# Kernel tuning notes

Hardware: AMD Instinct MI355X
Metric: run time of the kernel (lower is better)

The kernel has to match this reference:

```python
import jax, jax.numpy as jnp
import numpy as np

DIM = 1024
CTX_DIM = 768
H = 16


def setup_inputs() -> dict:
    key = jax.random.key(0)
    k1, k2, k3, k4, k5 = jax.random.split(key, 5)
    x = jax.random.normal(k1, (2, 2048, DIM), dtype=jnp.float32)
    context = jax.random.normal(k2, (2, 2048, CTX_DIM), dtype=jnp.float32)
    # Linear weights stored as [in, out] (y = x @ W); no biases per module.
    s = 0.02
    Wq = jax.random.normal(k3, (DIM, DIM), dtype=jnp.float32) * s
    Wkv = jax.random.normal(k4, (CTX_DIM, 2 * DIM), dtype=jnp.float32) * s
    Wo = jax.random.normal(k5, (DIM, DIM), dtype=jnp.float32) * s
    return {"x": x, "context": context, "Wq": Wq, "Wkv": Wkv, "Wo": Wo}


def reference(x, context, Wq, Wkv, Wo):
    B, N, C = x.shape
    Dh = C // H  # head dim
    scale = Dh ** -0.5
    M = context.shape[1]
    q = (x @ Wq).reshape(B, N, H, Dh).transpose(0, 2, 1, 3)      # [B,H,N,Dh]
    kv = context @ Wkv                                            # [B,M,2C]
    k, v = jnp.split(kv, 2, axis=-1)
    k = k.reshape(B, M, H, Dh).transpose(0, 2, 1, 3)              # [B,H,M,Dh]
    v = v.reshape(B, M, H, Dh).transpose(0, 2, 1, 3)              # [B,H,M,Dh]
    attn = jax.nn.softmax(jnp.einsum('bhnd,bhmd->bhnm', q, k) * scale, axis=-1)
    out = jnp.einsum('bhnm,bhmd->bhnd', attn, v)                  # [B,H,N,Dh]
    out = out.transpose(0, 2, 1, 3).reshape(B, N, C)
    return out @ Wo  # dropout is identity in eval / p=0
```

## Files before the change

### kernel.cpp

```cpp
#include <hip/hip_runtime.h>

typedef __attribute__((ext_vector_type(4))) float f32x4;
typedef __attribute__((ext_vector_type(8))) short short8;
typedef __attribute__((ext_vector_type(4))) unsigned int u32x4;
typedef unsigned short u16;
typedef unsigned int u32;
typedef unsigned long long u64;

__device__ __forceinline__ u16 f2bf(float f) {
  u32 u = __builtin_bit_cast(u32, f);
  u += 0x7fffu + ((u >> 16) & 1u);
  return (u16)(u >> 16);
}

__device__ __forceinline__ void gl2lds16(const u16* g, const u16* l) {
  __builtin_amdgcn_global_load_lds(
      (const __attribute__((address_space(1))) u32*)g,
      (__attribute__((address_space(3))) u32*)(u32)(u64)l,
      16, 0, 0);
}

__device__ __forceinline__ void cast_body(const float* __restrict__ s,
                                          u16* __restrict__ d, int blk,
                                          int tid) {
  long i = (long)blk * 256 + tid;
  const f32x4* sp = (const f32x4*)(s + i * 8);
  f32x4 a = sp[0], b = sp[1];
  u16 t[8];
#pragma unroll
  for (int j = 0; j < 4; j++) {
    t[j] = f2bf(a[j]);
    t[4 + j] = f2bf(b[j]);
  }
  *(u32x4*)(d + i * 8) = *(u32x4*)t;
}

__device__ __forceinline__ void transpose_body(const float* __restrict__ W,
                                               u16* __restrict__ WT, int K,
                                               int N, int k0, int n0, int tid,
                                               u16* T) {
#pragma unroll
  for (int i = 0; i < 4; i++) {
    int c = tid + 256 * i;
    int row = c >> 4;
    int ch = c & 15;
    f32x4 f = *(const f32x4*)(W + (long)(k0 + row) * N + n0 + ch * 4);
#pragma unroll
    for (int j = 0; j < 4; j++) T[(ch * 4 + j) * 72 + row] = f2bf(f[j]);
  }
  __syncthreads();
#pragma unroll
  for (int i = 0; i < 2; i++) {
    int c = tid + 256 * i;
    int row = c >> 3;
    int ch = c & 7;
    u32x4 v = *(u32x4*)&T[row * 72 + ch * 8];
    *(u32x4*)(WT + (long)(n0 + row) * K + k0 + ch * 8) = v;
  }
}

__global__ __launch_bounds__(256) void prep(
    const float* __restrict__ x, const float* __restrict__ ctx,
    const float* __restrict__ Wq, const float* __restrict__ Wkv,
    const float* __restrict__ Wo, u16* __restrict__ xb,
    u16* __restrict__ ctxb, u16* __restrict__ wqT, u16* __restrict__ wkvT,
    u16* __restrict__ woT) {
  __shared__ __align__(16) u16 T[64 * 72];
  const int b = blockIdx.x, tid = threadIdx.x;
  if (b < 2048) {
    cast_body(x, xb, b, tid);
  } else if (b < 3584) {
    cast_body(ctx, ctxb, b - 2048, tid);
  } else if (b < 3840) {
    int idx = b - 3584;
    transpose_body(Wq, wqT, 1024, 1024, (idx >> 4) * 64, (idx & 15) * 64, tid, T);
  } else if (b < 4224) {
    int idx = b - 3840;
    transpose_body(Wkv, wkvT, 768, 2048, (idx >> 5) * 64, (idx & 31) * 64, tid, T);
  } else {
    int idx = b - 4224;
    transpose_body(Wo, woT, 1024, 1024, (idx >> 4) * 64, (idx & 15) * 64, tid, T);
  }
}

__device__ __forceinline__ void gemm128_core(
    const u16* __restrict__ A, const u16* __restrict__ Bt, int Kstride,
    int Klen, long brow, long bcol, int tid, u16* As, u16* Bs,
    f32x4 (&acc)[4][4]) {
  const int lane = tid & 63, wv = tid >> 6;
  const int l15 = lane & 15, quad = lane >> 4;
  const int wr = (wv >> 1) * 64, wc = (wv & 1) * 64;
  const int sr = lane >> 3, sc = lane & 7;
  const int csw = ((sc ^ sr) & 7) * 8;

  const u16* ag[4];
  const u16* bg[4];
  const u16* al[4];
  const u16* bl[4];
#pragma unroll
  for (int n = 0; n < 4; n++) {
    int row = wv * 32 + n * 8;
    ag[n] = A + (brow + row + sr) * (long)Kstride + csw;
    al[n] = &As[row * 64];
    bg[n] = Bt + (bcol + row + sr) * (long)Kstride + csw;
    bl[n] = &Bs[row * 64];
  }

  for (int kt = 0; kt < Klen; kt += 64) {
    __syncthreads();
#pragma unroll
    for (int n = 0; n < 4; n++) gl2lds16(ag[n] + kt, al[n]);
#pragma unroll
    for (int n = 0; n < 4; n++) gl2lds16(bg[n] + kt, bl[n]);
    __syncthreads();
#pragma unroll
    for (int kk = 0; kk < 2; kk++) {
      short8 af[4], bf[4];
#pragma unroll
      for (int i = 0; i < 4; i++) {
        int row = wr + i * 16 + l15;
        af[i] = *(short8*)&As[row * 64 + (((kk * 4 + quad) ^ (row & 7)) << 3)];
      }
#pragma unroll
      for (int j = 0; j < 4; j++) {
        int row = wc + j * 16 + l15;
        bf[j] = *(short8*)&Bs[row * 64 + (((kk * 4 + quad) ^ (row & 7)) << 3)];
      }
#pragma unroll
      for (int i = 0; i < 4; i++)
#pragma unroll
        for (int j = 0; j < 4; j++)
          acc[i][j] = __builtin_amdgcn_mfma_f32_16x16x32_bf16(
              af[i], bf[j], acc[i][j], 0, 0, 0);
    }
  }
}

__global__ __launch_bounds__(256, 3) void fused_qkv(
    const u16* __restrict__ xb, const u16* __restrict__ ctxb,
    const u16* __restrict__ wqT, const u16* __restrict__ wkvT,
    u16* __restrict__ Qb, u16* __restrict__ Kfrag, u16* __restrict__ Vfrag,
    float qscale) {
  __shared__ __align__(16) u16 As[128 * 64];
  __shared__ __align__(16) u16 Bs[128 * 64];
  const int tid = threadIdx.x;
  const int lane = tid & 63, wv = tid >> 6;
  const int l15 = lane & 15, quad = lane >> 4;
  const int wr = (wv >> 1) * 64, wc = (wv & 1) * 64;

  f32x4 acc[4][4];
#pragma unroll
  for (int i = 0; i < 4; i++)
#pragma unroll
    for (int j = 0; j < 4; j++) acc[i][j] = (f32x4){0.f, 0.f, 0.f, 0.f};

  int bid = blockIdx.x;
  if (bid < 256) {
    long brow = (long)(bid >> 3) * 128, bcol = (long)(bid & 7) * 128;
    gemm128_core(xb, wqT, 1024, 1024, brow, bcol, tid, As, Bs, acc);
#pragma unroll
    for (int i = 0; i < 4; i++)
#pragma unroll
      for (int j = 0; j < 4; j++)
#pragma unroll
        for (int r = 0; r < 4; r++) {
          long row = brow + wr + i * 16 + quad * 4 + r;
          long col = bcol + wc + j * 16 + l15;
          Qb[row * 1024 + col] = f2bf(acc[i][j][r] * qscale);
        }
    return;
  }

  bid -= 256;
  long brow = (long)(bid >> 4) * 128, bcol = (long)(bid & 15) * 128;
  gemm128_core(ctxb, wkvT, 768, 768, brow, bcol, tid, As, Bs, acc);

  const bool is_k = (bcol < 1024);
  __syncthreads();
#pragma unroll
  for (int round = 0; round < 2; round++) {
    if ((wv >> 1) == round) {
      if (is_k) {
#pragma unroll
        for (int i = 0; i < 4; i++)
#pragma unroll
          for (int j = 0; j < 4; j++) {
            int d = j * 16 + l15;
            int off = (wv & 1) * 4096 + ((d >> 5) * 4 + i) * 512 +
                      (((d >> 3) & 3) * 16 + quad * 4) * 8 + (d & 7);
#pragma unroll
            for (int r = 0; r < 4; r++) As[off + r * 8] = f2bf(acc[i][j][r]);
          }
      } else {
#pragma unroll
        for (int i = 0; i < 4; i++)
#pragma unroll
          for (int j = 0; j < 4; j++) {
            int off = (wv & 1) * 4096 + ((i >> 1) * 4 + j) * 512 +
                      (quad * 16 + l15) * 8 + (i & 1) * 4;
            u16 t4[4];
#pragma unroll
            for (int r = 0; r < 4; r++) t4[r] = f2bf(acc[i][j][r]);
            *(u64*)&As[off] = *(const u64*)t4;
          }
      }
    }
    __syncthreads();
    long mg = brow + round * 64;
    int b_ = (int)(mg >> 11), mt = (int)((mg >> 6) & 31);
#pragma unroll
    for (int h2 = 0; h2 < 2; h2++) {
      int h = (int)((is_k ? bcol : bcol - 1024) >> 6) + h2;
      u16* dst = (is_k ? Kfrag : Vfrag) + ((long)(b_ * 16 + h) * 32 + mt) * 4096;
#pragma unroll
      for (int p = 0; p < 2; p++) {
        int c = p * 256 + tid;
        *(u32x4*)(dst + c * 8) = *(u32x4*)&As[h2 * 4096 + c * 8];
      }
    }
    __syncthreads();
  }
}

__global__ __launch_bounds__(256, 3) void gemm_o(
    const u16* __restrict__ A, const u16* __restrict__ Bt,
    float* __restrict__ C) {
  __shared__ __align__(16) u16 As[128 * 64];
  __shared__ __align__(16) u16 Bs[128 * 64];
  const int tid = threadIdx.x;
  const int lane = tid & 63, wv = tid >> 6;
  const int l15 = lane & 15, quad = lane >> 4;
  const int wr = (wv >> 1) * 64, wc = (wv & 1) * 64;
  long brow = (long)blockIdx.y * 128, bcol = (long)blockIdx.x * 128;

  f32x4 acc[4][4];
#pragma unroll
  for (int i = 0; i < 4; i++)
#pragma unroll
    for (int j = 0; j < 4; j++) acc[i][j] = (f32x4){0.f, 0.f, 0.f, 0.f};

  gemm128_core(A, Bt, 1024, 1024, brow, bcol, tid, As, Bs, acc);

#pragma unroll
  for (int i = 0; i < 4; i++)
#pragma unroll
    for (int j = 0; j < 4; j++)
#pragma unroll
      for (int r = 0; r < 4; r++) {
        long row = brow + wr + i * 16 + quad * 4 + r;
        long col = bcol + wc + j * 16 + l15;
        C[row * 1024 + col] = acc[i][j][r];
      }
}

__global__ __launch_bounds__(512, 4) void attn_kernel(
    const u16* __restrict__ Q, const u16* __restrict__ Kfrag,
    const u16* __restrict__ Vfrag, u16* __restrict__ AO) {
  __shared__ __align__(16) u16 smem[2][4][4096];
  const int tid = threadIdx.x;
  const int lane = tid & 63, wv = tid >> 6;
  const int qc = wv & 3, half = wv >> 2;
  const int l15 = lane & 15, quad = lane >> 4;
  const int bh = blockIdx.y;
  const int b = bh >> 4, h = bh & 15;
  const long qrow0 = (long)b * 2048 + blockIdx.x * 128 + qc * 32;

  short8 qf[2][2];
#pragma unroll
  for (int qt = 0; qt < 2; qt++)
#pragma unroll
    for (int kk = 0; kk < 2; kk++)
      qf[qt][kk] = *(const short8*)&Q[(qrow0 + qt * 16 + l15) * 1024 +
                                      h * 64 + kk * 32 + quad * 8];

  f32x4 O[2][5];
#pragma unroll
  for (int qt = 0; qt < 2; qt++)
#pragma unroll
    for (int dt = 0; dt < 5; dt++) O[qt][dt] = (f32x4){0.f, 0.f, 0.f, 0.f};

  u32x4 ones_u = {0x3F803F80u, 0x3F803F80u, 0x3F803F80u, 0x3F803F80u};
  short8 ones = __builtin_bit_cast(short8, ones_u);
  const f32x4 z4 = {0.f, 0.f, 0.f, 0.f};

  const u16* kg0 = Kfrag + (long)bh * 32 * 4096;
  const u16* vg0 = Vfrag + (long)bh * 32 * 4096;
  const int so = wv * 512 + lane * 8;

  auto stage = [&](int nb, int i) {
    const u16* k0 = kg0 + (long)i * 4096 + so;
    const u16* v0 = vg0 + (long)i * 4096 + so;
    gl2lds16(k0, &smem[nb][0][wv * 512]);
    gl2lds16(v0, &smem[nb][1][wv * 512]);
    gl2lds16(k0 + 16 * 4096, &smem[nb][2][wv * 512]);
    gl2lds16(v0 + 16 * 4096, &smem[nb][3][wv * 512]);
  };

  stage(0, 0);
  __syncthreads();

  for (int i = 0; i < 16; i++) {
    const int cur = i & 1;
    if (i < 15) stage(cur ^ 1, i + 1);

    const u16* Ks = &smem[cur][half * 2][0] + lane * 8;
    const u16* Vs = &smem[cur][half * 2 + 1][0] + lane * 8;

    f32x4 s[4][2];
    {
      short8 kf[4];
#pragma unroll
      for (int t = 0; t < 4; t++) kf[t] = *(const short8*)(Ks + t * 512);
      __builtin_amdgcn_s_setprio(1);
#pragma unroll
      for (int m4 = 0; m4 < 4; m4++)
#pragma unroll
        for (int qt = 0; qt < 2; qt++)
          s[m4][qt] = __builtin_amdgcn_mfma_f32_16x16x32_bf16(
              kf[m4], qf[qt][0], z4, 0, 0, 0);
      __builtin_amdgcn_s_setprio(0);
    }
    {
      short8 kf[4];
#pragma unroll
      for (int t = 0; t < 4; t++) kf[t] = *(const short8*)(Ks + (4 + t) * 512);
      __builtin_amdgcn_s_setprio(1);
#pragma unroll
      for (int m4 = 0; m4 < 4; m4++)
#pragma unroll
        for (int qt = 0; qt < 2; qt++)
          s[m4][qt] = __builtin_amdgcn_mfma_f32_16x16x32_bf16(
              kf[m4], qf[qt][1], s[m4][qt], 0, 0, 0);
      __builtin_amdgcn_s_setprio(0);
    }

#pragma unroll
    for (int kk = 0; kk < 2; kk++) {
      short8 vf[4];
#pragma unroll
      for (int dt = 0; dt < 4; dt++)
        vf[dt] = *(const short8*)(Vs + (kk * 4 + dt) * 512);
#pragma unroll
      for (int qt = 0; qt < 2; qt++) {
        u32 w[4];
#pragma unroll
        for (int hw = 0; hw < 2; hw++) {
          f32x4 sv = s[2 * kk + hw][qt];
          u32 e0 = __builtin_bit_cast(u32, __builtin_amdgcn_exp2f(sv[0]));
          u32 e1 = __builtin_bit_cast(u32, __builtin_amdgcn_exp2f(sv[1]));
          u32 e2 = __builtin_bit_cast(u32, __builtin_amdgcn_exp2f(sv[2]));
          u32 e3 = __builtin_bit_cast(u32, __builtin_amdgcn_exp2f(sv[3]));
          w[hw * 2] = __builtin_amdgcn_perm(e1, e0, 0x07060302u);
          w[hw * 2 + 1] = __builtin_amdgcn_perm(e3, e2, 0x07060302u);
        }
        short8 pa = __builtin_bit_cast(short8, *(u32x4*)w);
        __builtin_amdgcn_s_setprio(1);
#pragma unroll
        for (int dt = 0; dt < 4; dt++)
          O[qt][dt] = __builtin_amdgcn_mfma_f32_16x16x32_bf16(
              pa, vf[dt], O[qt][dt], 0, 0, 0);
        O[qt][4] = __builtin_amdgcn_mfma_f32_16x16x32_bf16(
            pa, ones, O[qt][4], 0, 0, 0);
        __builtin_amdgcn_s_setprio(0);
      }
    }
    __syncthreads();
  }

  f32x4* cb = (f32x4*)&smem[0][0][0];
  if (half) {
#pragma unroll
    for (int qt = 0; qt < 2; qt++)
#pragma unroll
      for (int dt = 0; dt < 5; dt++)
        cb[(qc * 64 + lane) * 10 + qt * 5 + dt] = O[qt][dt];
  }
  __syncthreads();
  if (!half) {
#pragma unroll
    for (int qt = 0; qt < 2; qt++)
#pragma unroll
      for (int dt = 0; dt < 5; dt++)
        O[qt][dt] += cb[(qc * 64 + lane) * 10 + qt * 5 + dt];

#pragma unroll
    for (int qt = 0; qt < 2; qt++) {
      float inv[4];
#pragma unroll
      for (int r = 0; r < 4; r++) inv[r] = 1.f / O[qt][4][r];
#pragma unroll
      for (int dt = 0; dt < 4; dt++)
#pragma unroll
        for (int r = 0; r < 4; r++) {
          long row = qrow0 + qt * 16 + quad * 4 + r;
          int col = h * 64 + dt * 16 + l15;
          AO[row * 1024 + col] = f2bf(O[qt][dt][r] * inv[r]);
        }
    }
  }
}

extern "C" void kernel_launch(void* const* d_in, const int* in_sizes, int n_in,
                              void* d_out, int out_size, void* d_ws,
                              size_t ws_size, hipStream_t stream) {
  const float* x = (const float*)d_in[0];
  const float* ctx = (const float*)d_in[1];
  const float* Wq = (const float*)d_in[2];
  const float* Wkv = (const float*)d_in[3];
  const float* Wo = (const float*)d_in[4];
  float* out = (float*)d_out;

  u16* ws = (u16*)d_ws;
  u16* wqT = ws;
  u16* wkvT = wqT + 1048576;
  u16* woT = wkvT + 1572864;
  u16* Qb = woT + 1048576;
  u16* Kfrag = Qb + 4194304;
  u16* Vfrag = Kfrag + 4194304;
  u16* xb = Vfrag + 4194304;
  u16* ctxb = xb + 4194304;
  u16* AOb = xb;

  const float qscale = 0.125f * 1.4426950408889634f;

  prep<<<dim3(4480), 256, 0, stream>>>(x, ctx, Wq, Wkv, Wo, xb, ctxb, wqT,
                                       wkvT, woT);

  fused_qkv<<<dim3(768), 256, 0, stream>>>(xb, ctxb, wqT, wkvT, Qb, Kfrag,
                                           Vfrag, qscale);

  attn_kernel<<<dim3(16, 32), 512, 0, stream>>>(Qb, Kfrag, Vfrag, AOb);

  gemm_o<<<dim3(8, 32), 256, 0, stream>>>(AOb, woT, out);
}
```

Measured before the change: 173.8 us.

## Fuse fp32-to-bf16 activation cast into QKV GEMM operand loading

New measurement: 186.0 us. 7.0% more time.

```diff
diff --git a/kernel.cpp b/kernel.cpp
--- a/kernel.cpp
+++ b/kernel.cpp
@@ -20,21 +20,6 @@
       16, 0, 0);
 }
 
-__device__ __forceinline__ void cast_body(const float* __restrict__ s,
-                                          u16* __restrict__ d, int blk,
-                                          int tid) {
-  long i = (long)blk * 256 + tid;
-  const f32x4* sp = (const f32x4*)(s + i * 8);
-  f32x4 a = sp[0], b = sp[1];
-  u16 t[8];
-#pragma unroll
-  for (int j = 0; j < 4; j++) {
-    t[j] = f2bf(a[j]);
-    t[4 + j] = f2bf(b[j]);
-  }
-  *(u32x4*)(d + i * 8) = *(u32x4*)t;
-}
-
 __device__ __forceinline__ void transpose_body(const float* __restrict__ W,
                                                u16* __restrict__ WT, int K,
                                                int N, int k0, int n0, int tid,
@@ -60,25 +45,18 @@
 }
 
 __global__ __launch_bounds__(256) void prep(
-    const float* __restrict__ x, const float* __restrict__ ctx,
     const float* __restrict__ Wq, const float* __restrict__ Wkv,
-    const float* __restrict__ Wo, u16* __restrict__ xb,
-    u16* __restrict__ ctxb, u16* __restrict__ wqT, u16* __restrict__ wkvT,
-    u16* __restrict__ woT) {
+    const float* __restrict__ Wo, u16* __restrict__ wqT,
+    u16* __restrict__ wkvT, u16* __restrict__ woT) {
   __shared__ __align__(16) u16 T[64 * 72];
   const int b = blockIdx.x, tid = threadIdx.x;
-  if (b < 2048) {
-    cast_body(x, xb, b, tid);
-  } else if (b < 3584) {
-    cast_body(ctx, ctxb, b - 2048, tid);
-  } else if (b < 3840) {
-    int idx = b - 3584;
-    transpose_body(Wq, wqT, 1024, 1024, (idx >> 4) * 64, (idx & 15) * 64, tid, T);
-  } else if (b < 4224) {
-    int idx = b - 3840;
+  if (b < 256) {
+    transpose_body(Wq, wqT, 1024, 1024, (b >> 4) * 64, (b & 15) * 64, tid, T);
+  } else if (b < 640) {
+    int idx = b - 256;
     transpose_body(Wkv, wkvT, 768, 2048, (idx >> 5) * 64, (idx & 31) * 64, tid, T);
   } else {
-    int idx = b - 4224;
+    int idx = b - 640;
     transpose_body(Wo, woT, 1024, 1024, (idx >> 4) * 64, (idx & 15) * 64, tid, T);
   }
 }
@@ -136,8 +114,75 @@
   }
 }
 
+__device__ __forceinline__ void gemm128_f32a(
+    const float* __restrict__ A, const u16* __restrict__ Bt, int Kstride,
+    int Klen, long brow, long bcol, int tid, u16* As, u16* Bs,
+    f32x4 (&acc)[4][4]) {
+  const int lane = tid & 63, wv = tid >> 6;
+  const int l15 = lane & 15, quad = lane >> 4;
+  const int wr = (wv >> 1) * 64, wc = (wv & 1) * 64;
+  const int sr = lane >> 3, sc = lane & 7;
+  const int csw = ((sc ^ sr) & 7) * 8;
+
+  const float* ag[4];
+  u16* alw[4];
+  const u16* bg[4];
+  const u16* bl[4];
+#pragma unroll
+  for (int n = 0; n < 4; n++) {
+    int row = wv * 32 + n * 8;
+    ag[n] = A + (brow + row + sr) * (long)Kstride + csw;
+    alw[n] = &As[row * 64 + lane * 8];
+    bg[n] = Bt + (bcol + row + sr) * (long)Kstride + csw;
+    bl[n] = &Bs[row * 64];
+  }
+
+  for (int kt = 0; kt < Klen; kt += 64) {
+    __syncthreads();
+#pragma unroll
+    for (int n = 0; n < 4; n++) gl2lds16(bg[n] + kt, bl[n]);
+    f32x4 a0[4], a1[4];
+#pragma unroll
+    for (int n = 0; n < 4; n++) {
+      a0[n] = *(const f32x4*)(ag[n] + kt);
+      a1[n] = *(const f32x4*)(ag[n] + kt + 4);
+    }
+#pragma unroll
+    for (int n = 0; n < 4; n++) {
+      u16 t[8];
+#pragma unroll
+      for (int j = 0; j < 4; j++) {
+        t[j] = f2bf(a0[n][j]);
+        t[4 + j] = f2bf(a1[n][j]);
+      }
+      *(u32x4*)alw[n] = *(u32x4*)t;
+    }
+    __syncthreads();
+#pragma unroll
+    for (int kk = 0; kk < 2; kk++) {
+      short8 af[4], bf[4];
+#pragma unroll
+      for (int i = 0; i < 4; i++) {
+        int row = wr + i * 16 + l15;
+        af[i] = *(short8*)&As[row * 64 + (((kk * 4 + quad) ^ (row & 7)) << 3)];
+      }
+#pragma unroll
+      for (int j = 0; j < 4; j++) {
+        int row = wc + j * 16 + l15;
+        bf[j] = *(short8*)&Bs[row * 64 + (((kk * 4 + quad) ^ (row & 7)) << 3)];
+      }
+#pragma unroll
+      for (int i = 0; i < 4; i++)
+#pragma unroll
+        for (int j = 0; j < 4; j++)
+          acc[i][j] = __builtin_amdgcn_mfma_f32_16x16x32_bf16(
+              af[i], bf[j], acc[i][j], 0, 0, 0);
+    }
+  }
+}
+
 __global__ __launch_bounds__(256, 3) void fused_qkv(
-    const u16* __restrict__ xb, const u16* __restrict__ ctxb,
+    const float* __restrict__ x, const float* __restrict__ ctx,
     const u16* __restrict__ wqT, const u16* __restrict__ wkvT,
     u16* __restrict__ Qb, u16* __restrict__ Kfrag, u16* __restrict__ Vfrag,
     float qscale) {
@@ -157,7 +202,7 @@
   int bid = blockIdx.x;
   if (bid < 256) {
     long brow = (long)(bid >> 3) * 128, bcol = (long)(bid & 7) * 128;
-    gemm128_core(xb, wqT, 1024, 1024, brow, bcol, tid, As, Bs, acc);
+    gemm128_f32a(x, wqT, 1024, 1024, brow, bcol, tid, As, Bs, acc);
 #pragma unroll
     for (int i = 0; i < 4; i++)
 #pragma unroll
@@ -173,7 +218,7 @@
 
   bid -= 256;
   long brow = (long)(bid >> 4) * 128, bcol = (long)(bid & 15) * 128;
-  gemm128_core(ctxb, wkvT, 768, 768, brow, bcol, tid, As, Bs, acc);
+  gemm128_f32a(ctx, wkvT, 768, 768, brow, bcol, tid, As, Bs, acc);
 
   const bool is_k = (bcol < 1024);
   __syncthreads();
@@ -417,16 +462,13 @@
   u16* Qb = woT + 1048576;
   u16* Kfrag = Qb + 4194304;
   u16* Vfrag = Kfrag + 4194304;
-  u16* xb = Vfrag + 4194304;
-  u16* ctxb = xb + 4194304;
-  u16* AOb = xb;
+  u16* AOb = Vfrag + 4194304;
 
   const float qscale = 0.125f * 1.4426950408889634f;
 
-  prep<<<dim3(4480), 256, 0, stream>>>(x, ctx, Wq, Wkv, Wo, xb, ctxb, wqT,
-                                       wkvT, woT);
-
-  fused_qkv<<<dim3(768), 256, 0, stream>>>(xb, ctxb, wqT, wkvT, Qb, Kfrag,
+  prep<<<dim3(896), 256, 0, stream>>>(Wq, Wkv, Wo, wqT, wkvT, woT);
+
+  fused_qkv<<<dim3(768), 256, 0, stream>>>(x, ctx, wqT, wkvT, Qb, Kfrag,
                                            Vfrag, qscale);
 
   attn_kernel<<<dim3(16, 32), 512, 0, stream>>>(Qb, Kfrag, Vfrag, AOb);
```

## Split K/V staging with finer vmcnt waits and swizzle attention block order

Applied to the files above, without the earlier changes.

New measurement: 171.5 us. Within noise of the previous version (-1.3%).

```diff
diff --git a/kernel.cpp b/kernel.cpp
--- a/kernel.cpp
+++ b/kernel.cpp
@@ -261,9 +261,12 @@
   const int lane = tid & 63, wv = tid >> 6;
   const int qc = wv & 3, half = wv >> 2;
   const int l15 = lane & 15, quad = lane >> 4;
-  const int bh = blockIdx.y;
+  const int bid0 = blockIdx.y * 16 + blockIdx.x;
+  const int nbid = (bid0 & 7) * 64 + (bid0 >> 3);
+  const int bh = nbid >> 4;
+  const int qt_ = nbid & 15;
   const int b = bh >> 4, h = bh & 15;
-  const long qrow0 = (long)b * 2048 + blockIdx.x * 128 + qc * 32;
+  const long qrow0 = (long)b * 2048 + qt_ * 128 + qc * 32;
 
   short8 qf[2][2];
 #pragma unroll
@@ -287,21 +290,27 @@
   const u16* vg0 = Vfrag + (long)bh * 32 * 4096;
   const int so = wv * 512 + lane * 8;
 
-  auto stage = [&](int nb, int i) {
+  auto stageK = [&](int nb, int i) {
     const u16* k0 = kg0 + (long)i * 4096 + so;
+    gl2lds16(k0, &smem[nb][0][wv * 512]);
+    gl2lds16(k0 + 16 * 4096, &smem[nb][2][wv * 512]);
+  };
+  auto stageV = [&](int nb, int i) {
     const u16* v0 = vg0 + (long)i * 4096 + so;
-    gl2lds16(k0, &smem[nb][0][wv * 512]);
     gl2lds16(v0, &smem[nb][1][wv * 512]);
-    gl2lds16(k0 + 16 * 4096, &smem[nb][2][wv * 512]);
     gl2lds16(v0 + 16 * 4096, &smem[nb][3][wv * 512]);
   };
 
-  stage(0, 0);
-  __syncthreads();
+  stageK(0, 0);
+  stageV(0, 0);
+  stageK(1, 1);
+  asm volatile("s_waitcnt vmcnt(2)" ::: "memory");
+  __builtin_amdgcn_s_barrier();
+  asm volatile("" ::: "memory");
 
   for (int i = 0; i < 16; i++) {
     const int cur = i & 1;
-    if (i < 15) stage(cur ^ 1, i + 1);
+    if (i + 1 < 16) stageV(cur ^ 1, i + 1);
 
     const u16* Ks = &smem[cur][half * 2][0] + lane * 8;
     const u16* Vs = &smem[cur][half * 2 + 1][0] + lane * 8;
@@ -333,6 +342,14 @@
               kf[m4], qf[qt][1], s[m4][qt], 0, 0, 0);
       __builtin_amdgcn_s_setprio(0);
     }
+
+    if (i < 15)
+      asm volatile("s_waitcnt vmcnt(4)" ::: "memory");
+    else
+      asm volatile("s_waitcnt vmcnt(0)" ::: "memory");
+    __builtin_amdgcn_s_barrier();
+    asm volatile("" ::: "memory");
+    if (i + 2 < 16) stageK(cur, i + 2);
 
 #pragma unroll
     for (int kk = 0; kk < 2; kk++) {
@@ -364,7 +381,15 @@
         __builtin_amdgcn_s_setprio(0);
       }
     }
-    __syncthreads();
+
+    if (i < 14)
+      asm volatile("s_waitcnt vmcnt(4)" ::: "memory");
+    else if (i == 14)
+      asm volatile("s_waitcnt vmcnt(2)" ::: "memory");
+    else
+      asm volatile("s_waitcnt vmcnt(0)" ::: "memory");
+    __builtin_amdgcn_s_barrier();
+    asm volatile("" ::: "memory");
   }
 
   f32x4* cb = (f32x4*)&smem[0][0][0];
```
